# Performance work log

Measured on AMD Instinct MI355X. Metric: run time of the kernel, lower is better.

The kernel has to match this reference:

```python
import jax, jax.numpy as jnp
import numpy as np

N_NODES = 50000
N_EDGES = 600000
N_GRAPHS = 2048
EMB = 128
N_LAYERS = 3
ATOM_FEATS, ATOM_VOCAB = 9, 100
BOND_FEATS, BOND_VOCAB, BOND_DIM = 3, 8, 3


def setup_inputs() -> dict:
    key = jax.random.key(0)
    ks = jax.random.split(key, 10)
    x = jax.random.randint(ks[0], (N_NODES, ATOM_FEATS), 0, ATOM_VOCAB)
    edge_index = jax.random.randint(ks[1], (2, N_EDGES), 0, N_NODES)
    edge_attr = jax.random.randint(ks[2], (N_EDGES, BOND_FEATS), 0, BOND_VOCAB)
    batch = jnp.sort(jax.random.randint(ks[3], (N_NODES,), 0, N_GRAPHS))
    s = 1.0 / np.sqrt(EMB).astype(np.float32)
    atom_emb = jax.random.normal(ks[4], (ATOM_FEATS, ATOM_VOCAB, EMB), jnp.float32) * 0.1
    bond_emb = jax.random.normal(ks[5], (N_LAYERS, BOND_FEATS, BOND_VOCAB, BOND_DIM), jnp.float32) * 0.1
    W = jax.random.normal(ks[6], (N_LAYERS, BOND_DIM, EMB, EMB), jnp.float32) * s
    b = jnp.zeros((N_LAYERS, BOND_DIM, EMB), jnp.float32)
    fc1_w = jax.random.normal(ks[7], (EMB, EMB), jnp.float32) * s
    fc1_b = jnp.zeros((EMB,), jnp.float32)
    fc2_w = jax.random.normal(ks[8], (EMB, 1), jnp.float32) * s
    fc2_b = jnp.zeros((1,), jnp.float32)
    return dict(x=x, edge_index=edge_index, edge_attr=edge_attr, batch=batch,
                atom_emb=atom_emb, bond_emb=bond_emb, W=W, b=b,
                fc1_w=fc1_w, fc1_b=fc1_b, fc2_w=fc2_w, fc2_b=fc2_b)


def reference(x, edge_index, edge_attr, batch, atom_emb, bond_emb, W, b,
              fc1_w, fc1_b, fc2_w, fc2_b):
    src, dst = edge_index[0], edge_index[1]
    n = x.shape[0]
    # AtomEncoder: sum of per-column embedding lookups -> [N, EMB]
    h = atom_emb[0][x[:, 0]]
    for c in range(1, ATOM_FEATS):
        h = h + atom_emb[c][x[:, c]]
    for layer in range(N_LAYERS):
        # BondEncoder: [E, BOND_DIM] edge weights (one scalar channel per conv)
        ew = bond_emb[layer, 0][edge_attr[:, 0]]
        for c in range(1, BOND_FEATS):
            ew = ew + bond_emb[layer, c][edge_attr[:, c]]
        # Three parallel GCNConv(normalize=False): linear, gather src, edge-weight, scatter-add to dst
        msg = jnp.zeros((edge_index.shape[1], EMB), h.dtype)
        for k in range(BOND_DIM):
            xw = h @ W[layer, k]              # [N, EMB]
            msg = msg + ew[:, k:k + 1] * xw[src]   # [E, EMB]
        agg = jax.ops.segment_sum(msg, dst, num_segments=n)
        hn = agg + jnp.sum(b[layer], axis=0)  # sum of the three conv biases
        if layer < N_LAYERS - 1:
            hn = jax.nn.relu(hn)              # dropout is identity at eval
        h = hn + h                            # residual
    # global_mean_pool
    sums = jax.ops.segment_sum(h, batch, num_segments=N_GRAPHS)
    counts = jax.ops.segment_sum(jnp.ones((n,), h.dtype), batch, num_segments=N_GRAPHS)
    hg = sums / jnp.maximum(counts, 1.0)[:, None]
    return (hg @ fc1_w + fc1_b) @ fc2_w + fc2_b   # [N_GRAPHS, 1]
```

## Files before the change

### kernel.cpp

```cpp
#include <hip/hip_runtime.h>

#define N_NODES 50000
#define N_EDGES 600000
#define N_GRAPHS 2048
#define EMB 128
#define TDIM 384
#define TS_LD 392
#define HN (N_NODES * EMB)
#define SCAN_NB ((N_NODES + 255) / 256)

#define PRE_ATOM_NB 8334
#define PRE_HIST_NB 1563
#define PRE_WCONV_NB 384
#define PRE_GB_NB 131

typedef __attribute__((ext_vector_type(8))) short bf16x8;
typedef __attribute__((ext_vector_type(4))) float f32x4;
#define MFMA_BF16(a, b, c) __builtin_amdgcn_mfma_f32_16x16x32_bf16(a, b, c, 0, 0, 0)

__device__ inline unsigned short f2bf(float f) {
  unsigned int u = __float_as_uint(f);
  u += 0x7fffu + ((u >> 16) & 1u);
  return (unsigned short)(u >> 16);
}
__device__ inline float bf2f(unsigned short b) {
  return __uint_as_float(((unsigned int)b) << 16);
}

__global__ __launch_bounds__(384) void k_pre(const int* __restrict__ x,
                                             const float* __restrict__ atom_emb,
                                             unsigned short* __restrict__ h_bf,
                                             const int* __restrict__ ei,
                                             int* __restrict__ deg,
                                             const float* __restrict__ W,
                                             unsigned short* __restrict__ wt,
                                             const int* __restrict__ batch,
                                             int* __restrict__ gs) {
  int blk = blockIdx.x;
  if (blk < PRE_ATOM_NB) {
    int n = blk * 6 + (threadIdx.x >> 6);
    int lane = threadIdx.x & 63;
    if (n < N_NODES) {
      const int nu = __builtin_amdgcn_readfirstlane(n);
      const int* xr = x + nu * 9;
      float2 acc = {0.f, 0.f};
#pragma unroll
      for (int c = 0; c < 9; ++c) {
        const float2* row = (const float2*)(atom_emb + (size_t)(c * 100 + xr[c]) * EMB);
        float2 v = row[lane];
        acc.x += v.x; acc.y += v.y;
      }
      *(ushort2*)(h_bf + (size_t)nu * EMB + lane * 2) = ushort2{f2bf(acc.x), f2bf(acc.y)};
    }
    return;
  }
  blk -= PRE_ATOM_NB;
  if (blk < PRE_HIST_NB) {
    int e = blk * 384 + threadIdx.x;
    if (e < N_EDGES) atomicAdd(&deg[ei[N_EDGES + e]], 1);
    return;
  }
  blk -= PRE_HIST_NB;
  if (blk < PRE_WCONV_NB) {
    int layer = blk >> 7, c = blk & 127, k = threadIdx.x;
    float v = W[(((layer * 3 + (k >> 7)) * 128) + (k & 127)) * 128 + c];
    wt[(size_t)blk * 384 + k] = f2bf(v);
    return;
  }
  blk -= PRE_WCONV_NB;
  {
    int i = blk * 384 + threadIdx.x;
    if (i < N_NODES) {
      int b = batch[i];
      int bp = (i == 0) ? -1 : batch[i - 1];
      for (int g = bp + 1; g <= b; ++g) gs[g] = i;
      if (i == N_NODES - 1) {
        for (int g = b + 1; g <= N_GRAPHS; ++g) gs[g] = N_NODES;
      }
    }
  }
}

__global__ __launch_bounds__(256) void k_scan_a(const int* __restrict__ deg,
                                                int* __restrict__ row_start,
                                                int* __restrict__ partials) {
  __shared__ int s[256];
  const int tid = threadIdx.x;
  const int i = blockIdx.x * 256 + tid;
  int v = (i < N_NODES) ? deg[i] : 0;
  s[tid] = v;
  __syncthreads();
  for (int off = 1; off < 256; off <<= 1) {
    int t = (tid >= off) ? s[tid - off] : 0;
    __syncthreads();
    s[tid] += t;
    __syncthreads();
  }
  if (i < N_NODES) row_start[i] = s[tid] - v;
  if (tid == 255) partials[blockIdx.x] = s[255];
}

__global__ __launch_bounds__(256) void k_scan_b(int* __restrict__ partials,
                                                int* __restrict__ row_start) {
  __shared__ int s[256];
  const int tid = threadIdx.x;
  int v = (tid < SCAN_NB) ? partials[tid] : 0;
  s[tid] = v;
  __syncthreads();
  for (int off = 1; off < 256; off <<= 1) {
    int t = (tid >= off) ? s[tid - off] : 0;
    __syncthreads();
    s[tid] += t;
    __syncthreads();
  }
  if (tid < SCAN_NB) partials[tid] = s[tid] - v;
  if (tid == 255) row_start[N_NODES] = s[255];
}

__global__ __launch_bounds__(256) void k_scan_c(int* __restrict__ row_start,
                                                const int* __restrict__ partials,
                                                int* __restrict__ cursor) {
  const int i = blockIdx.x * 256 + threadIdx.x;
  if (i < N_NODES) {
    int r = row_start[i] + partials[blockIdx.x];
    row_start[i] = r;
    cursor[i] = r;
  }
}

__global__ __launch_bounds__(256) void k_scatter(const int* __restrict__ ei,
                                                 const int* __restrict__ ea,
                                                 int* __restrict__ cursor,
                                                 int2* __restrict__ sorted_se) {
  int e = blockIdx.x * 256 + threadIdx.x;
  if (e >= N_EDGES) return;
  int src = ei[e], dst = ei[N_EDGES + e];
  int pos = atomicAdd(&cursor[dst], 1);
  int eap = ea[e * 3 + 0] | (ea[e * 3 + 1] << 3) | (ea[e * 3 + 2] << 6);
  sorted_se[pos] = int2{src, eap};
}

__global__ __launch_bounds__(256) void k_agg(const int2* __restrict__ sorted_se,
                                             const int* __restrict__ row_start,
                                             const float* __restrict__ bl,
                                             const unsigned short* __restrict__ h_bf,
                                             unsigned short* __restrict__ t_bf) {
  __shared__ float4 combo[512];
  for (int c = threadIdx.x; c < 512; c += 256) {
    int a0 = c & 7, a1 = (c >> 3) & 7, a2 = (c >> 6) & 7;
    combo[c] = float4{bl[a0 * 3 + 0] + bl[24 + a1 * 3 + 0] + bl[48 + a2 * 3 + 0],
                      bl[a0 * 3 + 1] + bl[24 + a1 * 3 + 1] + bl[48 + a2 * 3 + 1],
                      bl[a0 * 3 + 2] + bl[24 + a1 * 3 + 2] + bl[48 + a2 * 3 + 2], 0.f};
  }
  __syncthreads();
  const int node = blockIdx.x * 8 + (threadIdx.x >> 5);
  const int sub = threadIdx.x & 31;
  const int beg = row_start[node], end = row_start[node + 1];
  float4 a0 = {0.f, 0.f, 0.f, 0.f}, a1 = a0, a2 = a0;
  int e = beg;
  const int full_end = beg + ((end - beg) & ~7);
  for (; e < full_end; e += 8) {
    int2 se[8];
#pragma unroll
    for (int i = 0; i < 8; ++i) se[i] = sorted_se[e + i];
    ushort4 u[8];
#pragma unroll
    for (int i = 0; i < 8; ++i)
      u[i] = *(const ushort4*)(h_bf + (size_t)se[i].x * EMB + sub * 4);
#pragma unroll
    for (int i = 0; i < 8; ++i) {
      float4 w = combo[se[i].y];
      float4 vf = {bf2f(u[i].x), bf2f(u[i].y), bf2f(u[i].z), bf2f(u[i].w)};
      a0 += vf * w.x;
      a1 += vf * w.y;
      a2 += vf * w.z;
    }
  }
  if (e < end) {
    int2 se[8];
#pragma unroll
    for (int i = 0; i < 8; ++i) {
      int idx = e + i;
      se[i] = sorted_se[idx < end ? idx : end - 1];
    }
    ushort4 u[8];
#pragma unroll
    for (int i = 0; i < 8; ++i)
      u[i] = *(const ushort4*)(h_bf + (size_t)se[i].x * EMB + sub * 4);
#pragma unroll
    for (int i = 0; i < 8; ++i) {
      float4 w = (e + i < end) ? combo[se[i].y] : float4{0.f, 0.f, 0.f, 0.f};
      float4 vf = {bf2f(u[i].x), bf2f(u[i].y), bf2f(u[i].z), bf2f(u[i].w)};
      a0 += vf * w.x;
      a1 += vf * w.y;
      a2 += vf * w.z;
    }
  }
  size_t base = (size_t)node * TDIM + sub * 4;
  *(ushort4*)(t_bf + base)       = ushort4{f2bf(a0.x), f2bf(a0.y), f2bf(a0.z), f2bf(a0.w)};
  *(ushort4*)(t_bf + base + 128) = ushort4{f2bf(a1.x), f2bf(a1.y), f2bf(a1.z), f2bf(a1.w)};
  *(ushort4*)(t_bf + base + 256) = ushort4{f2bf(a2.x), f2bf(a2.y), f2bf(a2.z), f2bf(a2.w)};
}

__global__ __launch_bounds__(512) void k_gemm(const unsigned short* __restrict__ t_bf,
                                              const unsigned short* __restrict__ wt,
                                              const float* __restrict__ bl,
                                              const unsigned short* __restrict__ h_in_bf,
                                              unsigned short* __restrict__ h_out_bf,
                                              int do_relu) {
  __shared__ unsigned short ts[32 * TS_LD];
  const int nb = blockIdx.x * 32;
  for (int i = threadIdx.x; i < 32 * 48; i += 512) {
    int r = i / 48, cc = i % 48;
    bf16x8 v = {};
    int row = nb + r;
    if (row < N_NODES) v = *(const bf16x8*)(t_bf + (size_t)row * TDIM + cc * 8);
    *(bf16x8*)(ts + r * TS_LD + cc * 8) = v;
  }
  __syncthreads();

  const int wv = threadIdx.x >> 6;
  const int lane = threadIdx.x & 63;
  const int m = lane & 15;
  const int kq = lane >> 4;
  const int c = wv * 16 + m;

  const unsigned short* pB = wt + (size_t)c * TDIM + kq * 8;
  bf16x8 B[12];
#pragma unroll
  for (int kc = 0; kc < 12; ++kc) B[kc] = *(const bf16x8*)(pB + kc * 32);

  const float bias = bl[c] + bl[128 + c] + bl[256 + c];

#pragma unroll
  for (int rt = 0; rt < 2; ++rt) {
    const unsigned short* pA = ts + (rt * 16 + m) * TS_LD + kq * 8;
    bf16x8 A[12];
#pragma unroll
    for (int kc = 0; kc < 12; ++kc) A[kc] = *(const bf16x8*)(pA + kc * 32);
    f32x4 acc = {0.f, 0.f, 0.f, 0.f};
#pragma unroll
    for (int kc = 0; kc < 12; ++kc) acc = MFMA_BF16(A[kc], B[kc], acc);
#pragma unroll
    for (int r = 0; r < 4; ++r) {
      int row = nb + rt * 16 + kq * 4 + r;
      if (row < N_NODES) {
        size_t idx = (size_t)row * EMB + c;
        float v = acc[r] + bias;
        if (do_relu) v = fmaxf(v, 0.f);
        float hn = bf2f(h_in_bf[idx]) + v;
        h_out_bf[idx] = f2bf(hn);
      }
    }
  }
}

__global__ __launch_bounds__(128) void k_head(const unsigned short* __restrict__ h_bf,
                                              const int* __restrict__ gs,
                                              const float* __restrict__ fc1_w,
                                              const float* __restrict__ fc1_b,
                                              const float* __restrict__ fc2_w,
                                              const float* __restrict__ fc2_b,
                                              float* __restrict__ out) {
  __shared__ float hg[EMB];
  __shared__ float red[EMB];
  int g = blockIdx.x, e = threadIdx.x;
  int ns = gs[g], ne = gs[g + 1];
  float acc = 0.f;
  for (int n = ns; n < ne; ++n) acc += bf2f(h_bf[(size_t)n * EMB + e]);
  float cnt = fmaxf((float)(ne - ns), 1.f);
  hg[e] = acc / cnt;
  __syncthreads();
  float a2 = fc1_b[e];
  for (int j = 0; j < EMB; ++j) a2 += hg[j] * fc1_w[j * EMB + e];
  red[e] = a2 * fc2_w[e];
  __syncthreads();
  for (int s = 64; s > 0; s >>= 1) {
    if (e < s) red[e] += red[e + s];
    __syncthreads();
  }
  if (e == 0) out[g] = red[0] + fc2_b[0];
}

extern "C" void kernel_launch(void* const* d_in, const int* in_sizes, int n_in,
                              void* d_out, int out_size, void* d_ws, size_t ws_size,
                              hipStream_t stream) {
  const int*   x        = (const int*)d_in[0];
  const int*   ei       = (const int*)d_in[1];
  const int*   ea       = (const int*)d_in[2];
  const int*   batch    = (const int*)d_in[3];
  const float* atom_emb = (const float*)d_in[4];
  const float* bond_emb = (const float*)d_in[5];
  const float* W        = (const float*)d_in[6];
  const float* b        = (const float*)d_in[7];
  const float* fc1_w    = (const float*)d_in[8];
  const float* fc1_b    = (const float*)d_in[9];
  const float* fc2_w    = (const float*)d_in[10];
  const float* fc2_b    = (const float*)d_in[11];
  float* out = (float*)d_out;

  char* p = (char*)d_ws;
  auto alloc = [&](size_t bytes) { char* r = p; p += (bytes + 255) & ~(size_t)255; return r; };
  unsigned short* h0_bf      = (unsigned short*)alloc((size_t)HN * 2);
  unsigned short* h1_bf      = (unsigned short*)alloc((size_t)HN * 2);
  unsigned short* t_bf       = (unsigned short*)alloc((size_t)N_NODES * TDIM * 2);
  unsigned short* wt         = (unsigned short*)alloc((size_t)3 * 128 * TDIM * 2);
  int*            gs         = (int*)alloc((size_t)(N_GRAPHS + 1) * 4);
  int*            deg        = (int*)alloc((size_t)N_NODES * 4);
  int*            row_start  = (int*)alloc((size_t)(N_NODES + 1) * 4);
  int*            cursor     = (int*)alloc((size_t)N_NODES * 4);
  int*            partials   = (int*)alloc(256 * 4);
  int2*           sorted_se  = (int2*)alloc((size_t)(N_EDGES + 8) * 8);

  hipMemsetAsync(deg, 0, N_NODES * sizeof(int), stream);
  const int pre_blocks = PRE_ATOM_NB + PRE_HIST_NB + PRE_WCONV_NB + PRE_GB_NB;
  k_pre<<<pre_blocks, 384, 0, stream>>>(x, atom_emb, h0_bf, ei, deg, W, wt, batch, gs);
  k_scan_a<<<SCAN_NB, 256, 0, stream>>>(deg, row_start, partials);
  k_scan_b<<<1, 256, 0, stream>>>(partials, row_start);
  k_scan_c<<<SCAN_NB, 256, 0, stream>>>(row_start, partials, cursor);
  k_scatter<<<(N_EDGES + 255) / 256, 256, 0, stream>>>(ei, ea, cursor, sorted_se);

  unsigned short* hib = h0_bf;
  unsigned short* hob = h1_bf;
  const int gemm_blocks = (N_NODES + 31) / 32;
  for (int layer = 0; layer < 3; ++layer) {
    k_agg<<<N_NODES / 8, 256, 0, stream>>>(sorted_se, row_start, bond_emb + layer * 72,
                                           hib, t_bf);
    k_gemm<<<gemm_blocks, 512, 0, stream>>>(
        t_bf, wt + (size_t)layer * 128 * TDIM, b + layer * 3 * EMB,
        hib, hob, layer < 2 ? 1 : 0);
    unsigned short* tb = hib; hib = hob; hob = tb;
  }

  k_head<<<N_GRAPHS, 128, 0, stream>>>(hib, gs, fc1_w, fc1_b, fc2_w, fc2_b, out);
}
```

Baseline: 370.1 us.

## Fuse edge aggregation into the GEMM kernel via shared-memory staging

Merges the per-layer aggregation and GEMM kernels into one. Each block now aggregates 32 nodes straight into its shared-memory tile and then runs the MFMA GEMM on that tile, so the global t_bf round trip and one launch per layer disappear. The weight fragments are loaded before the aggregation, which raises register pressure, and the gather now runs in 512-thread blocks that hold more LDS per block. The atom encoder separately loads all nine indices and rows before summing, to expose more memory-level parallelism.

```diff
diff --git a/kernel.cpp b/kernel.cpp
--- a/kernel.cpp
+++ b/kernel.cpp
@@ -43,13 +43,16 @@
     if (n < N_NODES) {
       const int nu = __builtin_amdgcn_readfirstlane(n);
       const int* xr = x + nu * 9;
+      int ix[9];
+#pragma unroll
+      for (int c = 0; c < 9; ++c) ix[c] = xr[c];
+      float2 v[9];
+#pragma unroll
+      for (int c = 0; c < 9; ++c)
+        v[c] = ((const float2*)(atom_emb + (size_t)(c * 100 + ix[c]) * EMB))[lane];
       float2 acc = {0.f, 0.f};
 #pragma unroll
-      for (int c = 0; c < 9; ++c) {
-        const float2* row = (const float2*)(atom_emb + (size_t)(c * 100 + xr[c]) * EMB);
-        float2 v = row[lane];
-        acc.x += v.x; acc.y += v.y;
-      }
+      for (int c = 0; c < 9; ++c) { acc.x += v[c].x; acc.y += v[c].y; }
       *(ushort2*)(h_bf + (size_t)nu * EMB + lane * 2) = ushort2{f2bf(acc.x), f2bf(acc.y)};
     }
     return;
@@ -140,97 +143,93 @@
   sorted_se[pos] = int2{src, eap};
 }
 
-__global__ __launch_bounds__(256) void k_agg(const int2* __restrict__ sorted_se,
-                                             const int* __restrict__ row_start,
-                                             const float* __restrict__ bl,
-                                             const unsigned short* __restrict__ h_bf,
-                                             unsigned short* __restrict__ t_bf) {
+__global__ __launch_bounds__(512) void k_fused(const int2* __restrict__ sorted_se,
+                                               const int* __restrict__ row_start,
+                                               const float* __restrict__ bl,
+                                               const unsigned short* __restrict__ wt,
+                                               const float* __restrict__ bb,
+                                               const unsigned short* __restrict__ h_in_bf,
+                                               unsigned short* __restrict__ h_out_bf,
+                                               int do_relu) {
   __shared__ float4 combo[512];
-  for (int c = threadIdx.x; c < 512; c += 256) {
-    int a0 = c & 7, a1 = (c >> 3) & 7, a2 = (c >> 6) & 7;
-    combo[c] = float4{bl[a0 * 3 + 0] + bl[24 + a1 * 3 + 0] + bl[48 + a2 * 3 + 0],
-                      bl[a0 * 3 + 1] + bl[24 + a1 * 3 + 1] + bl[48 + a2 * 3 + 1],
-                      bl[a0 * 3 + 2] + bl[24 + a1 * 3 + 2] + bl[48 + a2 * 3 + 2], 0.f};
-  }
-  __syncthreads();
-  const int node = blockIdx.x * 8 + (threadIdx.x >> 5);
-  const int sub = threadIdx.x & 31;
-  const int beg = row_start[node], end = row_start[node + 1];
-  float4 a0 = {0.f, 0.f, 0.f, 0.f}, a1 = a0, a2 = a0;
-  int e = beg;
-  const int full_end = beg + ((end - beg) & ~7);
-  for (; e < full_end; e += 8) {
-    int2 se[8];
-#pragma unroll
-    for (int i = 0; i < 8; ++i) se[i] = sorted_se[e + i];
-    ushort4 u[8];
-#pragma unroll
-    for (int i = 0; i < 8; ++i)
-      u[i] = *(const ushort4*)(h_bf + (size_t)se[i].x * EMB + sub * 4);
-#pragma unroll
-    for (int i = 0; i < 8; ++i) {
-      float4 w = combo[se[i].y];
-      float4 vf = {bf2f(u[i].x), bf2f(u[i].y), bf2f(u[i].z), bf2f(u[i].w)};
-      a0 += vf * w.x;
-      a1 += vf * w.y;
-      a2 += vf * w.z;
-    }
-  }
-  if (e < end) {
-    int2 se[8];
-#pragma unroll
-    for (int i = 0; i < 8; ++i) {
-      int idx = e + i;
-      se[i] = sorted_se[idx < end ? idx : end - 1];
-    }
-    ushort4 u[8];
-#pragma unroll
-    for (int i = 0; i < 8; ++i)
-      u[i] = *(const ushort4*)(h_bf + (size_t)se[i].x * EMB + sub * 4);
-#pragma unroll
-    for (int i = 0; i < 8; ++i) {
-      float4 w = (e + i < end) ? combo[se[i].y] : float4{0.f, 0.f, 0.f, 0.f};
-      float4 vf = {bf2f(u[i].x), bf2f(u[i].y), bf2f(u[i].z), bf2f(u[i].w)};
-      a0 += vf * w.x;
-      a1 += vf * w.y;
-      a2 += vf * w.z;
-    }
-  }
-  size_t base = (size_t)node * TDIM + sub * 4;
-  *(ushort4*)(t_bf + base)       = ushort4{f2bf(a0.x), f2bf(a0.y), f2bf(a0.z), f2bf(a0.w)};
-  *(ushort4*)(t_bf + base + 128) = ushort4{f2bf(a1.x), f2bf(a1.y), f2bf(a1.z), f2bf(a1.w)};
-  *(ushort4*)(t_bf + base + 256) = ushort4{f2bf(a2.x), f2bf(a2.y), f2bf(a2.z), f2bf(a2.w)};
-}
-
-__global__ __launch_bounds__(512) void k_gemm(const unsigned short* __restrict__ t_bf,
-                                              const unsigned short* __restrict__ wt,
-                                              const float* __restrict__ bl,
-                                              const unsigned short* __restrict__ h_in_bf,
-                                              unsigned short* __restrict__ h_out_bf,
-                                              int do_relu) {
   __shared__ unsigned short ts[32 * TS_LD];
-  const int nb = blockIdx.x * 32;
-  for (int i = threadIdx.x; i < 32 * 48; i += 512) {
-    int r = i / 48, cc = i % 48;
-    bf16x8 v = {};
-    int row = nb + r;
-    if (row < N_NODES) v = *(const bf16x8*)(t_bf + (size_t)row * TDIM + cc * 8);
-    *(bf16x8*)(ts + r * TS_LD + cc * 8) = v;
-  }
-  __syncthreads();
-
-  const int wv = threadIdx.x >> 6;
-  const int lane = threadIdx.x & 63;
+  const int tid = threadIdx.x;
+
+  {
+    int a0 = tid & 7, a1 = (tid >> 3) & 7, a2 = (tid >> 6) & 7;
+    combo[tid] = float4{bl[a0 * 3 + 0] + bl[24 + a1 * 3 + 0] + bl[48 + a2 * 3 + 0],
+                        bl[a0 * 3 + 1] + bl[24 + a1 * 3 + 1] + bl[48 + a2 * 3 + 1],
+                        bl[a0 * 3 + 2] + bl[24 + a1 * 3 + 2] + bl[48 + a2 * 3 + 2], 0.f};
+  }
+
+  const int wv = tid >> 6;
+  const int lane = tid & 63;
   const int m = lane & 15;
   const int kq = lane >> 4;
   const int c = wv * 16 + m;
-
   const unsigned short* pB = wt + (size_t)c * TDIM + kq * 8;
   bf16x8 B[12];
 #pragma unroll
   for (int kc = 0; kc < 12; ++kc) B[kc] = *(const bf16x8*)(pB + kc * 32);
-
-  const float bias = bl[c] + bl[128 + c] + bl[256 + c];
+  const float bias = bb[c] + bb[128 + c] + bb[256 + c];
+
+  __syncthreads();
+
+  const int hw = tid >> 5;
+  const int sub = tid & 31;
+  const int nb = blockIdx.x * 32;
+#pragma unroll
+  for (int i = 0; i < 2; ++i) {
+    const int node = nb + i * 16 + hw;
+    float4 a0 = {0.f, 0.f, 0.f, 0.f}, a1 = a0, a2 = a0;
+    if (node < N_NODES) {
+      const int beg = row_start[node], end = row_start[node + 1];
+      int e = beg;
+      const int full_end = beg + ((end - beg) & ~7);
+      for (; e < full_end; e += 8) {
+        int2 se[8];
+#pragma unroll
+        for (int j = 0; j < 8; ++j) se[j] = sorted_se[e + j];
+        ushort4 u[8];
+#pragma unroll
+        for (int j = 0; j < 8; ++j)
+          u[j] = *(const ushort4*)(h_in_bf + (size_t)se[j].x * EMB + sub * 4);
+#pragma unroll
+        for (int j = 0; j < 8; ++j) {
+          float4 w = combo[se[j].y];
+          float4 vf = {bf2f(u[j].x), bf2f(u[j].y), bf2f(u[j].z), bf2f(u[j].w)};
+          a0 += vf * w.x;
+          a1 += vf * w.y;
+          a2 += vf * w.z;
+        }
+      }
+      if (e < end) {
+        int2 se[8];
+#pragma unroll
+        for (int j = 0; j < 8; ++j) {
+          int idx = e + j;
+          se[j] = sorted_se[idx < end ? idx : end - 1];
+        }
+        ushort4 u[8];
+#pragma unroll
+        for (int j = 0; j < 8; ++j)
+          u[j] = *(const ushort4*)(h_in_bf + (size_t)se[j].x * EMB + sub * 4);
+#pragma unroll
+        for (int j = 0; j < 8; ++j) {
+          float4 w = (e + j < end) ? combo[se[j].y] : float4{0.f, 0.f, 0.f, 0.f};
+          float4 vf = {bf2f(u[j].x), bf2f(u[j].y), bf2f(u[j].z), bf2f(u[j].w)};
+          a0 += vf * w.x;
+          a1 += vf * w.y;
+          a2 += vf * w.z;
+        }
+      }
+    }
+    size_t base = (size_t)(i * 16 + hw) * TS_LD + sub * 4;
+    *(ushort4*)(ts + base)       = ushort4{f2bf(a0.x), f2bf(a0.y), f2bf(a0.z), f2bf(a0.w)};
+    *(ushort4*)(ts + base + 128) = ushort4{f2bf(a1.x), f2bf(a1.y), f2bf(a1.z), f2bf(a1.w)};
+    *(ushort4*)(ts + base + 256) = ushort4{f2bf(a2.x), f2bf(a2.y), f2bf(a2.z), f2bf(a2.w)};
+  }
+  __syncthreads();
 
 #pragma unroll
   for (int rt = 0; rt < 2; ++rt) {
@@ -303,7 +302,6 @@
   auto alloc = [&](size_t bytes) { char* r = p; p += (bytes + 255) & ~(size_t)255; return r; };
   unsigned short* h0_bf      = (unsigned short*)alloc((size_t)HN * 2);
   unsigned short* h1_bf      = (unsigned short*)alloc((size_t)HN * 2);
-  unsigned short* t_bf       = (unsigned short*)alloc((size_t)N_NODES * TDIM * 2);
   unsigned short* wt         = (unsigned short*)alloc((size_t)3 * 128 * TDIM * 2);
   int*            gs         = (int*)alloc((size_t)(N_GRAPHS + 1) * 4);
   int*            deg        = (int*)alloc((size_t)N_NODES * 4);
@@ -322,12 +320,11 @@
 
   unsigned short* hib = h0_bf;
   unsigned short* hob = h1_bf;
-  const int gemm_blocks = (N_NODES + 31) / 32;
+  const int fused_blocks = (N_NODES + 31) / 32;
   for (int layer = 0; layer < 3; ++layer) {
-    k_agg<<<N_NODES / 8, 256, 0, stream>>>(sorted_se, row_start, bond_emb + layer * 72,
-                                           hib, t_bf);
-    k_gemm<<<gemm_blocks, 512, 0, stream>>>(
-        t_bf, wt + (size_t)layer * 128 * TDIM, b + layer * 3 * EMB,
+    k_fused<<<fused_blocks, 512, 0, stream>>>(
+        sorted_se, row_start, bond_emb + layer * 72,
+        wt + (size_t)layer * 128 * TDIM, b + layer * 3 * EMB,
         hib, hob, layer < 2 ? 1 : 0);
     unsigned short* tb = hib; hib = hob; hob = tb;
   }
```

Result: slower. 435.0 us (+17.5%).
